# Kernel tuning notes

Measured on AMD Instinct MI355X. Metric: run time of the kernel, lower is better.

The kernel has to match this reference:

```python
import jax, jax.numpy as jnp
import numpy as np
from jax import lax

B, T, I, H = 32, 512, 256, 512


def setup_inputs() -> dict:
    key = jax.random.key(0)
    ks = jax.random.split(key, 6)
    s_ih = 1.0 / np.sqrt(I)
    s_hh = 1.0 / np.sqrt(H)
    return {
        "x": jax.random.normal(ks[0], (B, T, I), dtype=jnp.float32),
        "W_ih_f": jax.random.normal(ks[1], (4 * H, I), dtype=jnp.float32) * s_ih,
        "W_hh_f": jax.random.normal(ks[2], (4 * H, H), dtype=jnp.float32) * s_hh,
        "b_f": jnp.zeros((4 * H,), dtype=jnp.float32),
        "W_ih_b": jax.random.normal(ks[3], (4 * H, I), dtype=jnp.float32) * s_ih,
        "W_hh_b": jax.random.normal(ks[4], (4 * H, H), dtype=jnp.float32) * s_hh,
        "b_b": jnp.zeros((4 * H,), dtype=jnp.float32),
    }


def _lstm(x, W_ih, W_hh, b):
    # x: [B, T, I] -> hidden sequence [B, T, H]
    Bx, Tx, _ = x.shape
    Hh = W_hh.shape[1]
    # precompute input projections for all timesteps: [T, B, 4H]
    x_proj = jnp.einsum('bti,gi->tbg', x, W_ih) + b

    def step(carry, xp):
        h, c = carry
        gates = xp + h @ W_hh.T  # [B, 4H]
        i, f, g, o = jnp.split(gates, 4, axis=-1)
        i = jax.nn.sigmoid(i)
        f = jax.nn.sigmoid(f)
        g = jnp.tanh(g)
        o = jax.nn.sigmoid(o)
        c = f * c + i * g
        h = o * jnp.tanh(c)
        return (h, c), h

    h0 = jnp.zeros((Bx, Hh), dtype=x.dtype)
    c0 = jnp.zeros((Bx, Hh), dtype=x.dtype)
    _, hs = lax.scan(step, (h0, c0), x_proj)  # hs: [T, B, H]
    return hs.transpose(1, 0, 2)


def reference(x, W_ih_f, W_hh_f, b_f, W_ih_b, W_hh_b, b_b):
    out_fwd = _lstm(x, W_ih_f, W_hh_f, b_f)                      # [B, T, H]
    x_rev = jnp.flip(x, axis=1)
    out_bwd = jnp.flip(_lstm(x_rev, W_ih_b, W_hh_b, b_b), axis=1)  # [B, T, H]
    return jnp.concatenate((out_fwd, out_bwd), axis=2)           # [B, T, 2H]
```

## Files before the change

### kernel.cpp

```cpp
#include <hip/hip_runtime.h>

#define B_    32
#define T_    512
#define I_    256
#define H_    512
#define PB    16
#define NBLK  32
#define NT    256
#define NSLOT 4
#define HPITCH 34

typedef __attribute__((ext_vector_type(8))) short  short8;
typedef __attribute__((ext_vector_type(4))) float  float4v;

__device__ __forceinline__ unsigned short f2bf(float f) {
    union { float f; unsigned u; } v; v.f = f;
    unsigned r = v.u + 0x7FFFu + ((v.u >> 16) & 1u);
    return (unsigned short)(r >> 16);
}

__device__ __forceinline__ short8 cvt8(const float* p) {
    float4 u = *reinterpret_cast<const float4*>(p);
    float4 v = *reinterpret_cast<const float4*>(p + 4);
    short8 r;
    r[0] = (short)f2bf(u.x); r[1] = (short)f2bf(u.y);
    r[2] = (short)f2bf(u.z); r[3] = (short)f2bf(u.w);
    r[4] = (short)f2bf(v.x); r[5] = (short)f2bf(v.y);
    r[6] = (short)f2bf(v.z); r[7] = (short)f2bf(v.w);
    return r;
}

__device__ __forceinline__ unsigned long long pack4bf(float a, float b, float c, float d) {
    return (unsigned long long)f2bf(a)
         | ((unsigned long long)f2bf(b) << 16)
         | ((unsigned long long)f2bf(c) << 32)
         | ((unsigned long long)f2bf(d) << 48);
}

__device__ __forceinline__ float sigm(float v)  { return 1.0f / (1.0f + __expf(-v)); }
__device__ __forceinline__ float tanhf_(float v){ return 2.0f / (1.0f + __expf(-2.0f * v)) - 1.0f; }

__global__ __launch_bounds__(256) void build_xfrag(const float* __restrict__ x,
                                                   unsigned short* __restrict__ xf) {
    const int t = blockIdx.x, tid = threadIdx.x;
#pragma unroll
    for (int rep = 0; rep < 4; ++rep) {
        const int eidx  = rep * 256 + tid;
        const int chunk = eidx >> 6, lf = eidx & 63;
        const int kstep = chunk >> 1, nh = chunk & 1;
        const int kq = lf >> 4, nm = lf & 15;
        const int b  = nh * 16 + nm;
        const int i0 = kstep * 32 + kq * 8;
        short8 v = cvt8(x + ((size_t)b * T_ + t) * I_ + i0);
        *reinterpret_cast<short8*>(xf + ((size_t)t * 16 + chunk) * 512 + lf * 8) = v;
    }
}

__global__ __launch_bounds__(NT, 1) void bilstm_mfma(
    const float* __restrict__ Wih_f, const float* __restrict__ Whh_f, const float* __restrict__ bias_f,
    const float* __restrict__ Wih_b, const float* __restrict__ Whh_b, const float* __restrict__ bias_b,
    float* __restrict__ out, float* __restrict__ ws) {

    __shared__ __align__(16) char  sAX[16 * 1024];
    __shared__ __align__(16) char  sAH[32 * 1024];
    __shared__ __align__(16) float sHT[B_ * HPITCH];

    const int tid  = threadIdx.x;
    const int lane = tid & 63;
    const int w    = tid >> 6;
    const int d    = blockIdx.x & 1;
    const int pb   = blockIdx.x >> 1;

    const char* xfrag_b = (const char*)ws;
    unsigned long long* hfrag = (unsigned long long*)((char*)ws + (size_t)T_ * 16 * 1024);
    const char* hfrag_b = (const char*)hfrag;
    unsigned* flags = (unsigned*)((char*)hfrag + (size_t)2 * NSLOT * 32 * 1024);

    const float* Wih = d ? Wih_b : Wih_f;
    const float* Whh = d ? Whh_b : Whh_f;
    const float* bia = d ? bias_b : bias_f;

    const int mA  = lane & 15;
    const int kqA = lane >> 4;
    const int gA  = mA & 3;
    const int gr0 = gA * H_ + 32 * pb + 8 * w + (mA >> 2);
    const int gr1 = gr0 + 4;

    short8 wx0[8], wx1[8], wh0[16], wh1[16];
#pragma unroll
    for (int kst = 0; kst < 8; ++kst) {
        wx0[kst] = cvt8(Wih + (size_t)gr0 * I_ + kst * 32 + kqA * 8);
        wx1[kst] = cvt8(Wih + (size_t)gr1 * I_ + kst * 32 + kqA * 8);
    }
#pragma unroll
    for (int kst = 0; kst < 16; ++kst) {
        wh0[kst] = cvt8(Whh + (size_t)gr0 * H_ + kst * 32 + kqA * 8);
        wh1[kst] = cvt8(Whh + (size_t)gr1 * H_ + kst * 32 + kqA * 8);
    }

    const int hid0 = 32 * pb + 8 * w + kqA;
    float4v bq0, bq1;
#pragma unroll
    for (int g = 0; g < 4; ++g) {
        bq0[g] = bia[g * H_ + hid0];
        bq1[g] = bia[g * H_ + hid0 + 4];
    }

    const int pub_b  = tid & 31;
    const int pub_r8 = tid >> 5;
    const unsigned pub_chunkL = pb * 2 + (pub_b >> 4);
    const unsigned pub_lf     = pub_r8 * 16 + (pub_b & 15);

    const unsigned* watch = flags + (d * 16 + (lane & 15)) * 16;
    unsigned* myflag      = flags + (d * 16 + pb) * 16;

    {
        const int tx0 = d ? (T_ - 1) : 0;
        const char* src = xfrag_b + ((size_t)tx0 * 16 + w * 4) * 1024 + lane * 16;
#pragma unroll
        for (int c = 0; c < 4; ++c) {
            uint4 v = *reinterpret_cast<const uint4*>(src + c * 1024);
            *reinterpret_cast<uint4*>(sAX + (w * 4 + c) * 1024 + lane * 16) = v;
        }
    }
    __syncthreads();

    float4v xa00 = bq0, xa01 = bq0, xa10 = bq1, xa11 = bq1;
#pragma unroll
    for (int kst = 0; kst < 8; ++kst) {
        short8 f0 = *reinterpret_cast<const short8*>(sAX + (kst * 2 + 0) * 1024 + lane * 16);
        short8 f1 = *reinterpret_cast<const short8*>(sAX + (kst * 2 + 1) * 1024 + lane * 16);
        xa00 = __builtin_amdgcn_mfma_f32_16x16x32_bf16(wx0[kst], f0, xa00, 0, 0, 0);
        xa01 = __builtin_amdgcn_mfma_f32_16x16x32_bf16(wx0[kst], f1, xa01, 0, 0, 0);
        xa10 = __builtin_amdgcn_mfma_f32_16x16x32_bf16(wx1[kst], f0, xa10, 0, 0, 0);
        xa11 = __builtin_amdgcn_mfma_f32_16x16x32_bf16(wx1[kst], f1, xa11, 0, 0, 0);
    }

    uint4 xpre[4];
    {
        const int tx1 = d ? (T_ - 2) : 1;
        const char* src = xfrag_b + ((size_t)tx1 * 16 + w * 4) * 1024 + lane * 16;
#pragma unroll
        for (int c = 0; c < 4; ++c)
            xpre[c] = *reinterpret_cast<const uint4*>(src + c * 1024);
    }

    float c00 = 0.f, c01 = 0.f, c10 = 0.f, c11 = 0.f;

    for (int t = 0; t < T_; ++t) {
        const int tx    = d ? (T_ - 1 - t) : t;
        const int slot  = t & (NSLOT - 1);
        const int pslot = (t - 1) & (NSLOT - 1);

        if (t > 0 && w == 0) {
            for (;;) {
                unsigned v = __hip_atomic_load(watch, __ATOMIC_RELAXED, __HIP_MEMORY_SCOPE_AGENT);
                if (__all(v >= (unsigned)t)) break;
                __builtin_amdgcn_s_sleep(1);
            }
        }
        __syncthreads();

        unsigned long long hbuf[16];
        if (t > 0) {
            const char* src = hfrag_b + ((size_t)(d * NSLOT + pslot) * 32 + w * 8) * 1024 + lane * 16;
#pragma unroll
            for (int c = 0; c < 8; ++c) {
                hbuf[2 * c + 0] = __hip_atomic_load((const unsigned long long*)(src + c * 1024),
                                                    __ATOMIC_RELAXED, __HIP_MEMORY_SCOPE_AGENT);
                hbuf[2 * c + 1] = __hip_atomic_load((const unsigned long long*)(src + c * 1024 + 8),
                                                    __ATOMIC_RELAXED, __HIP_MEMORY_SCOPE_AGENT);
            }
#pragma unroll
            for (int c = 0; c < 8; ++c) {
                char* dst = sAH + (w * 8 + c) * 1024 + lane * 16;
                *reinterpret_cast<unsigned long long*>(dst)     = hbuf[2 * c + 0];
                *reinterpret_cast<unsigned long long*>(dst + 8) = hbuf[2 * c + 1];
            }
        }
        __syncthreads();

        float4v a00 = xa00, a01 = xa01, a10 = xa10, a11 = xa11;

        if (t > 0) {
#pragma unroll
            for (int kst = 0; kst < 16; ++kst) {
                short8 f0 = *reinterpret_cast<const short8*>(sAH + (kst * 2 + 0) * 1024 + lane * 16);
                short8 f1 = *reinterpret_cast<const short8*>(sAH + (kst * 2 + 1) * 1024 + lane * 16);
                a00 = __builtin_amdgcn_mfma_f32_16x16x32_bf16(wh0[kst], f0, a00, 0, 0, 0);
                a01 = __builtin_amdgcn_mfma_f32_16x16x32_bf16(wh0[kst], f1, a01, 0, 0, 0);
                a10 = __builtin_amdgcn_mfma_f32_16x16x32_bf16(wh1[kst], f0, a10, 0, 0, 0);
                a11 = __builtin_amdgcn_mfma_f32_16x16x32_bf16(wh1[kst], f1, a11, 0, 0, 0);
            }
        }

        float h00, h01, h10, h11;
        {
            float iv, fv, gv, ov, c;
            iv = sigm(a00[0]); fv = sigm(a00[1]); gv = tanhf_(a00[2]); ov = sigm(a00[3]);
            c = fv * c00 + iv * gv; c00 = c; h00 = ov * tanhf_(c);
            iv = sigm(a01[0]); fv = sigm(a01[1]); gv = tanhf_(a01[2]); ov = sigm(a01[3]);
            c = fv * c01 + iv * gv; c01 = c; h01 = ov * tanhf_(c);
            iv = sigm(a10[0]); fv = sigm(a10[1]); gv = tanhf_(a10[2]); ov = sigm(a10[3]);
            c = fv * c10 + iv * gv; c10 = c; h10 = ov * tanhf_(c);
            iv = sigm(a11[0]); fv = sigm(a11[1]); gv = tanhf_(a11[2]); ov = sigm(a11[3]);
            c = fv * c11 + iv * gv; c11 = c; h11 = ov * tanhf_(c);
        }

        {
            const int hl = 8 * w + kqA;
            const int bn = mA;
            sHT[(bn)      * HPITCH + hl]     = h00;
            sHT[(bn + 16) * HPITCH + hl]     = h01;
            sHT[(bn)      * HPITCH + hl + 4] = h10;
            sHT[(bn + 16) * HPITCH + hl + 4] = h11;
        }
        __syncthreads();

        float2 f01, f23, f45, f67;
        if (tid < 128) {
            const float* rp = sHT + pub_b * HPITCH + 8 * pub_r8;
            f01 = *reinterpret_cast<const float2*>(rp + 0);
            f23 = *reinterpret_cast<const float2*>(rp + 2);
            f45 = *reinterpret_cast<const float2*>(rp + 4);
            f67 = *reinterpret_cast<const float2*>(rp + 6);
            const unsigned long long lo = pack4bf(f01.x, f01.y, f23.x, f23.y);
            const unsigned long long hi = pack4bf(f45.x, f45.y, f67.x, f67.y);
            char* dst = (char*)hfrag + ((size_t)((d * NSLOT + slot) * 32 + pub_chunkL)) * 1024
                      + pub_lf * 16;
            __hip_atomic_store((unsigned long long*)dst,       lo, __ATOMIC_RELAXED, __HIP_MEMORY_SCOPE_AGENT);
            __hip_atomic_store((unsigned long long*)(dst + 8), hi, __ATOMIC_RELAXED, __HIP_MEMORY_SCOPE_AGENT);
        }
        __syncthreads();

        if (tid == 0)
            __hip_atomic_store(myflag, (unsigned)(t + 1), __ATOMIC_RELAXED,
                               __HIP_MEMORY_SCOPE_AGENT);

        if (tid < 128) {
            float* op = out + ((size_t)pub_b * T_ + tx) * (2 * H_) + (size_t)d * H_
                      + 32 * pb + 8 * pub_r8;
            *reinterpret_cast<float4*>(op + 0) = make_float4(f01.x, f01.y, f23.x, f23.y);
            *reinterpret_cast<float4*>(op + 4) = make_float4(f45.x, f45.y, f67.x, f67.y);
        }

        if (t + 1 < T_) {
#pragma unroll
            for (int c = 0; c < 4; ++c)
                *reinterpret_cast<uint4*>(sAX + (w * 4 + c) * 1024 + lane * 16) = xpre[c];

            if (t + 2 < T_) {
                const int txn2 = d ? (T_ - 3 - t) : (t + 2);
                const char* src = xfrag_b + ((size_t)txn2 * 16 + w * 4) * 1024 + lane * 16;
#pragma unroll
                for (int c = 0; c < 4; ++c)
                    xpre[c] = *reinterpret_cast<const uint4*>(src + c * 1024);
            }
            __syncthreads();

            xa00 = bq0; xa01 = bq0; xa10 = bq1; xa11 = bq1;
#pragma unroll
            for (int kst = 0; kst < 8; ++kst) {
                short8 f0 = *reinterpret_cast<const short8*>(sAX + (kst * 2 + 0) * 1024 + lane * 16);
                short8 f1 = *reinterpret_cast<const short8*>(sAX + (kst * 2 + 1) * 1024 + lane * 16);
                xa00 = __builtin_amdgcn_mfma_f32_16x16x32_bf16(wx0[kst], f0, xa00, 0, 0, 0);
                xa01 = __builtin_amdgcn_mfma_f32_16x16x32_bf16(wx0[kst], f1, xa01, 0, 0, 0);
                xa10 = __builtin_amdgcn_mfma_f32_16x16x32_bf16(wx1[kst], f0, xa10, 0, 0, 0);
                xa11 = __builtin_amdgcn_mfma_f32_16x16x32_bf16(wx1[kst], f1, xa11, 0, 0, 0);
            }
        }
    }
}

extern "C" void kernel_launch(void* const* d_in, const int* in_sizes, int n_in,
                              void* d_out, int out_size, void* d_ws, size_t ws_size,
                              hipStream_t stream) {
    const float* x     = (const float*)d_in[0];
    const float* Wih_f = (const float*)d_in[1];
    const float* Whh_f = (const float*)d_in[2];
    const float* b_f   = (const float*)d_in[3];
    const float* Wih_b = (const float*)d_in[4];
    const float* Whh_b = (const float*)d_in[5];
    const float* b_b   = (const float*)d_in[6];
    float* out = (float*)d_out;

    const size_t xf_bytes  = (size_t)T_ * 16 * 1024;
    const size_t hf_bytes  = (size_t)2 * NSLOT * 32 * 1024;
    const size_t flag_bytes = (size_t)2 * 16 * 16 * sizeof(unsigned);

    hipMemsetAsync((char*)d_ws + xf_bytes + hf_bytes, 0, flag_bytes, stream);

    hipLaunchKernelGGL(build_xfrag, dim3(T_), dim3(256), 0, stream,
                       x, (unsigned short*)d_ws);

    hipLaunchKernelGGL(bilstm_mfma, dim3(NBLK), dim3(NT), 0, stream,
                       Wih_f, Whh_f, b_f, Wih_b, Whh_b, b_b, out, (float*)d_ws);
}
```

Measured before the change: 2.475 ms.

## Replace syncthreads with raw barriers and split publish/output across waves

Replaces __syncthreads with raw s_barrier plus explicit waitcnt and sched barriers, and removes the barrier between the hidden-state publish and the flag store by using a release store on the flag. The publish of bf16 h fragments is packed into one wave, while waves 2-3 write the fp32 output concurrently. The x-fragment LDS buffer is double-buffered so the next step's staging does not conflict with readers. This aims to shorten the per-timestep critical path of the recurrent cross-block handoff, at the cost of relying on hand-placed waitcnts and release ordering for correctness.

```diff
diff --git a/kernel.cpp b/kernel.cpp
--- a/kernel.cpp
+++ b/kernel.cpp
@@ -40,6 +40,22 @@
 __device__ __forceinline__ float sigm(float v)  { return 1.0f / (1.0f + __expf(-v)); }
 __device__ __forceinline__ float tanhf_(float v){ return 2.0f / (1.0f + __expf(-2.0f * v)) - 1.0f; }
 
+__device__ __forceinline__ void bar_raw() {
+    __builtin_amdgcn_sched_barrier(0);
+    asm volatile("" ::: "memory");
+    __builtin_amdgcn_s_barrier();
+    asm volatile("" ::: "memory");
+    __builtin_amdgcn_sched_barrier(0);
+}
+__device__ __forceinline__ void wait_lgkm0() {
+    asm volatile("s_waitcnt lgkmcnt(0)" ::: "memory");
+    __builtin_amdgcn_sched_barrier(0);
+}
+__device__ __forceinline__ void wait_vm0() {
+    asm volatile("s_waitcnt vmcnt(0)" ::: "memory");
+    __builtin_amdgcn_sched_barrier(0);
+}
+
 __global__ __launch_bounds__(256) void build_xfrag(const float* __restrict__ x,
                                                    unsigned short* __restrict__ xf) {
     const int t = blockIdx.x, tid = threadIdx.x;
@@ -61,7 +77,7 @@
     const float* __restrict__ Wih_b, const float* __restrict__ Whh_b, const float* __restrict__ bias_b,
     float* __restrict__ out, float* __restrict__ ws) {
 
-    __shared__ __align__(16) char  sAX[16 * 1024];
+    __shared__ __align__(16) char  sAX[2 * 16 * 1024];
     __shared__ __align__(16) char  sAH[32 * 1024];
     __shared__ __align__(16) float sHT[B_ * HPITCH];
 
@@ -105,11 +121,6 @@
         bq0[g] = bia[g * H_ + hid0];
         bq1[g] = bia[g * H_ + hid0 + 4];
     }
-
-    const int pub_b  = tid & 31;
-    const int pub_r8 = tid >> 5;
-    const unsigned pub_chunkL = pb * 2 + (pub_b >> 4);
-    const unsigned pub_lf     = pub_r8 * 16 + (pub_b & 15);
 
     const unsigned* watch = flags + (d * 16 + (lane & 15)) * 16;
     unsigned* myflag      = flags + (d * 16 + pb) * 16;
@@ -159,10 +170,10 @@
                 __builtin_amdgcn_s_sleep(1);
             }
         }
-        __syncthreads();
-
-        unsigned long long hbuf[16];
+        bar_raw();
+
         if (t > 0) {
+            unsigned long long hbuf[16];
             const char* src = hfrag_b + ((size_t)(d * NSLOT + pslot) * 32 + w * 8) * 1024 + lane * 16;
 #pragma unroll
             for (int c = 0; c < 8; ++c) {
@@ -171,14 +182,16 @@
                 hbuf[2 * c + 1] = __hip_atomic_load((const unsigned long long*)(src + c * 1024 + 8),
                                                     __ATOMIC_RELAXED, __HIP_MEMORY_SCOPE_AGENT);
             }
+            wait_vm0();
 #pragma unroll
             for (int c = 0; c < 8; ++c) {
                 char* dst = sAH + (w * 8 + c) * 1024 + lane * 16;
                 *reinterpret_cast<unsigned long long*>(dst)     = hbuf[2 * c + 0];
                 *reinterpret_cast<unsigned long long*>(dst + 8) = hbuf[2 * c + 1];
             }
-        }
-        __syncthreads();
+            wait_lgkm0();
+        }
+        bar_raw();
 
         float4v a00 = xa00, a01 = xa01, a10 = xa10, a11 = xa11;
 
@@ -215,39 +228,48 @@
             sHT[(bn)      * HPITCH + hl + 4] = h10;
             sHT[(bn + 16) * HPITCH + hl + 4] = h11;
         }
-        __syncthreads();
-
-        float2 f01, f23, f45, f67;
-        if (tid < 128) {
-            const float* rp = sHT + pub_b * HPITCH + 8 * pub_r8;
-            f01 = *reinterpret_cast<const float2*>(rp + 0);
-            f23 = *reinterpret_cast<const float2*>(rp + 2);
-            f45 = *reinterpret_cast<const float2*>(rp + 4);
-            f67 = *reinterpret_cast<const float2*>(rp + 6);
-            const unsigned long long lo = pack4bf(f01.x, f01.y, f23.x, f23.y);
-            const unsigned long long hi = pack4bf(f45.x, f45.y, f67.x, f67.y);
-            char* dst = (char*)hfrag + ((size_t)((d * NSLOT + slot) * 32 + pub_chunkL)) * 1024
-                      + pub_lf * 16;
-            __hip_atomic_store((unsigned long long*)dst,       lo, __ATOMIC_RELAXED, __HIP_MEMORY_SCOPE_AGENT);
-            __hip_atomic_store((unsigned long long*)(dst + 8), hi, __ATOMIC_RELAXED, __HIP_MEMORY_SCOPE_AGENT);
-        }
-        __syncthreads();
-
+        wait_lgkm0();
+        bar_raw();
+
+        if (tid < 64) {
+            const int b     = lane & 31;
+            const int rbase = (lane >> 5) * 2;
+#pragma unroll
+            for (int j = 0; j < 2; ++j) {
+                const int r8 = rbase + j;
+                const float* rp = sHT + b * HPITCH + 8 * r8;
+                const unsigned long long lo = pack4bf(rp[0], rp[1], rp[2], rp[3]);
+                const unsigned long long hi = pack4bf(rp[4], rp[5], rp[6], rp[7]);
+                const unsigned chunkL = pb * 2 + (b >> 4);
+                const unsigned lf     = r8 * 16 + (b & 15);
+                char* dst = (char*)hfrag + ((size_t)((d * NSLOT + slot) * 32 + chunkL)) * 1024
+                          + lf * 16;
+                __hip_atomic_store((unsigned long long*)dst,       lo, __ATOMIC_RELAXED, __HIP_MEMORY_SCOPE_AGENT);
+                __hip_atomic_store((unsigned long long*)(dst + 8), hi, __ATOMIC_RELAXED, __HIP_MEMORY_SCOPE_AGENT);
+            }
+        }
         if (tid == 0)
-            __hip_atomic_store(myflag, (unsigned)(t + 1), __ATOMIC_RELAXED,
+            __hip_atomic_store(myflag, (unsigned)(t + 1), __ATOMIC_RELEASE,
                                __HIP_MEMORY_SCOPE_AGENT);
-
-        if (tid < 128) {
-            float* op = out + ((size_t)pub_b * T_ + tx) * (2 * H_) + (size_t)d * H_
-                      + 32 * pb + 8 * pub_r8;
-            *reinterpret_cast<float4*>(op + 0) = make_float4(f01.x, f01.y, f23.x, f23.y);
-            *reinterpret_cast<float4*>(op + 4) = make_float4(f45.x, f45.y, f67.x, f67.y);
+        __builtin_amdgcn_sched_barrier(0);
+
+        if (tid >= 128) {
+            const int ob  = tid & 31;
+            const int or8 = (tid >> 5) & 3;
+            const float* rp = sHT + ob * HPITCH + 8 * or8;
+            float4 v0 = make_float4(rp[0], rp[1], rp[2], rp[3]);
+            float4 v1 = make_float4(rp[4], rp[5], rp[6], rp[7]);
+            float* op = out + ((size_t)ob * T_ + tx) * (2 * H_) + (size_t)d * H_
+                      + 32 * pb + 8 * or8;
+            *reinterpret_cast<float4*>(op + 0) = v0;
+            *reinterpret_cast<float4*>(op + 4) = v1;
         }
 
         if (t + 1 < T_) {
+            char* xb = sAX + ((t + 1) & 1) * 16384;
 #pragma unroll
             for (int c = 0; c < 4; ++c)
-                *reinterpret_cast<uint4*>(sAX + (w * 4 + c) * 1024 + lane * 16) = xpre[c];
+                *reinterpret_cast<uint4*>(xb + (w * 4 + c) * 1024 + lane * 16) = xpre[c];
 
             if (t + 2 < T_) {
                 const int txn2 = d ? (T_ - 3 - t) : (t + 2);
@@ -256,13 +278,14 @@
                 for (int c = 0; c < 4; ++c)
                     xpre[c] = *reinterpret_cast<const uint4*>(src + c * 1024);
             }
-            __syncthreads();
+            wait_lgkm0();
+            bar_raw();
 
             xa00 = bq0; xa01 = bq0; xa10 = bq1; xa11 = bq1;
 #pragma unroll
             for (int kst = 0; kst < 8; ++kst) {
-                short8 f0 = *reinterpret_cast<const short8*>(sAX + (kst * 2 + 0) * 1024 + lane * 16);
-                short8 f1 = *reinterpret_cast<const short8*>(sAX + (kst * 2 + 1) * 1024 + lane * 16);
+                short8 f0 = *reinterpret_cast<const short8*>(xb + (kst * 2 + 0) * 1024 + lane * 16);
+                short8 f1 = *reinterpret_cast<const short8*>(xb + (kst * 2 + 1) * 1024 + lane * 16);
                 xa00 = __builtin_amdgcn_mfma_f32_16x16x32_bf16(wx0[kst], f0, xa00, 0, 0, 0);
                 xa01 = __builtin_amdgcn_mfma_f32_16x16x32_bf16(wx0[kst], f1, xa01, 0, 0, 0);
                 xa10 = __builtin_amdgcn_mfma_f32_16x16x32_bf16(wx1[kst], f0, xa10, 0, 0, 0);
@@ -284,8 +307,8 @@
     const float* b_b   = (const float*)d_in[6];
     float* out = (float*)d_out;
 
-    const size_t xf_bytes  = (size_t)T_ * 16 * 1024;
-    const size_t hf_bytes  = (size_t)2 * NSLOT * 32 * 1024;
+    const size_t xf_bytes   = (size_t)T_ * 16 * 1024;
+    const size_t hf_bytes   = (size_t)2 * NSLOT * 32 * 1024;
     const size_t flag_bytes = (size_t)2 * 16 * 16 * sizeof(unsigned);
 
     hipMemsetAsync((char*)d_ws + xf_bytes + hf_bytes, 0, flag_bytes, stream);
```

Result: slower. 2.841 ms (+14.8%).
